# Performance work log

Hardware: AMD Instinct MI355X
Metric: run time of the kernel (lower is better)

The kernel has to match this reference:

```python
import jax, jax.numpy as jnp
import numpy as np
import math

B, S, HID = 2, 2048, 512
H, HKV, QB, VB = 8, 2, 8, 16
W = 256 // QB            # suffix window size = 32
QKD = W * QB             # unfolded qk dim = 256
TAU = 1.0


def setup_inputs() -> dict:
    key = jax.random.key(0)
    ks = jax.random.split(key, 7)
    return {
        "hidden_states": jax.random.normal(ks[0], (B, S, HID), jnp.float32),
        "Wq": jax.random.normal(ks[1], (H * QB, HID), jnp.float32) * (HID ** -0.5),
        "Wk": jax.random.normal(ks[2], (HKV * QB, HID), jnp.float32) * (HID ** -0.5),
        "Wv": jax.random.normal(ks[3], (HKV * VB, HID), jnp.float32) * (HID ** -0.5),
        "Wo": jax.random.normal(ks[4], (HID, H * VB), jnp.float32) * ((H * VB) ** -0.5),
        "v_emb0": jnp.full((H * VB,), -1e-5, jnp.float32),
        "v_emb1": jnp.full((H * VB,), +1e-5, jnp.float32),
    }


def _forward(hidden_states, Wq, Wk, Wv, Wo, v_emb0, v_emb1):
    b, s, _ = hidden_states.shape
    # bit-quantized (soft) q/k/v projections
    q = jnp.tanh((hidden_states @ Wq.T) / TAU).reshape(b, s, H, QB).transpose(0, 2, 1, 3)      # [B,H,S,QB]
    k = jnp.tanh((hidden_states @ Wk.T) / TAU).reshape(b, s, HKV, QB).transpose(0, 2, 1, 3)    # [B,HKV,S,QB]
    v = jax.nn.sigmoid((hidden_states @ Wv.T) / TAU).reshape(b, s, HKV, VB).transpose(0, 2, 1, 3)
    # suffix shift of values: F.pad(v, (0,0,-1,1)) -> v[t] <- v[t+1], last position zero
    v = jnp.concatenate([v[:, :, 1:], jnp.zeros_like(v[:, :, :1])], axis=2)                    # [B,HKV,S,VB]
    # left-pad seq by W-1 zeros, then unfold sliding windows of length W
    pad = ((0, 0), (0, 0), (W - 1, 0), (0, 0))
    qp, kp = jnp.pad(q, pad), jnp.pad(k, pad)
    win = jnp.arange(s)[:, None] + jnp.arange(W)[None, :]   # [S,W] window indices into padded seq
    qw = qp[:, :, win, :].reshape(b, H, s, QKD)             # concat window positions x bits
    kw = kp[:, :, win, :].reshape(b, HKV, s, QKD)
    # GQA: repeat kv heads
    rep = H // HKV
    kw = jnp.repeat(kw, rep, axis=1)
    vr = jnp.repeat(v, rep, axis=1)
    scale = 1.0 / math.sqrt(QKD) / TAU
    # custom bias r_j / (r_i + 1) under strictly-causal mask (j < i)
    r = jnp.arange(s, dtype=hidden_states.dtype)
    mask = jnp.tril(jnp.ones((s, s), dtype=bool), -1)
    bias = jnp.where(mask, (r[None, :] / (r[:, None] + 1.0)) / TAU, 0.0)
    scores = jnp.einsum('bhqd,bhkd->bhqk', qw, kw) * scale + bias
    neg = jnp.finfo(scores.dtype).min
    scores = jnp.where(mask, scores, neg)
    # stable masked softmax (fully-masked row 0 -> zero weights instead of NaN)
    scores = scores - jax.lax.stop_gradient(jnp.max(scores, axis=-1, keepdims=True))
    e = jnp.exp(scores) * mask
    attn = e / jnp.maximum(jnp.sum(e, axis=-1, keepdims=True), 1e-30)
    out = jnp.einsum('bhqk,bhkd->bhqd', attn, vr)           # [B,H,S,VB]
    out = out.transpose(0, 2, 1, 3).reshape(b, s, H * VB)
    # learned emb0/emb1 interpolation
    out = out * v_emb1 + (1.0 - out) * v_emb0
    return out @ Wo.T


def reference(hidden_states, Wq, Wk, Wv, Wo, v_emb0, v_emb1):
    return _forward(hidden_states, Wq, Wk, Wv, Wo, v_emb0, v_emb1)
```

## Files before the change

### kernel.cpp

```cpp
#include <hip/hip_runtime.h>
#include <hip/hip_bf16.h>

typedef unsigned int u32;
typedef unsigned short u16;
typedef float f32x4 __attribute__((ext_vector_type(4)));
typedef short s16x8 __attribute__((ext_vector_type(8)));

#define B_   2
#define S_   2048
#define HID_ 512
#define H_   8
#define HKV_ 2
#define QB_  8
#define VB_  16
#define NQ_  64
#define HVB_ 128
#define SCALE_ 0.0625f
#define MFIX_  17.0f

__device__ __forceinline__ u16 f2bf(float f) {
    u32 b = __builtin_bit_cast(u32, f);
    b += 0x7FFFu + ((b >> 16) & 1u);
    return (u16)(b >> 16);
}
__device__ __forceinline__ float bf2f(u16 h) {
    u32 b = ((u32)h) << 16;
    return __builtin_bit_cast(float, b);
}
__device__ __forceinline__ f32x4 mfma16(s16x8 a, s16x8 b, f32x4 c) {
    return __builtin_amdgcn_mfma_f32_16x16x32_bf16(a, b, c, 0, 0, 0);
}
__device__ __forceinline__ float fast_tanh(float x) {
    float e = __expf(2.f * x);
    return 1.f - 2.f * __builtin_amdgcn_rcpf(e + 1.f);
}
__device__ __forceinline__ float fast_sigmoid(float x) {
    return __builtin_amdgcn_rcpf(1.f + __expf(-x));
}

__global__ void k0_convert(const float* __restrict__ Wq, const float* __restrict__ Wk,
                           const float* __restrict__ Wv, const float* __restrict__ Wo,
                           u16* __restrict__ Wc, u16* __restrict__ Wob) {
    int idx = blockIdx.x * 256 + threadIdx.x;
    {
        int n = idx >> 9, k = idx & 511;
        float v = (n < NQ_) ? Wq[n * HID_ + k]
                : (n < NQ_ + 16) ? Wk[(n - NQ_) * HID_ + k]
                : (n < 112) ? Wv[(n - NQ_ - 16) * HID_ + k] : 0.f;
        Wc[idx] = f2bf(v);
    }
    Wob[idx] = f2bf(Wo[idx]);
}

__global__ __launch_bounds__(256) void k1_proj(
    const float* __restrict__ hidden, const u16* __restrict__ Wc,
    u16* __restrict__ qb, u16* __restrict__ kb, u16* __restrict__ vt)
{
    const int tid = threadIdx.x;
    const int r0 = blockIdx.x * 16;
    const int wv = tid >> 6, lane = tid & 63;
    const int li = lane & 15, lo4 = lane >> 4;

    const float* hrow = hidden + (r0 + li) * HID_;

    f32x4 acc[2];
    acc[0] = (f32x4){0.f, 0.f, 0.f, 0.f};
    acc[1] = (f32x4){0.f, 0.f, 0.f, 0.f};

    #pragma unroll
    for (int kc = 0; kc < 16; ++kc) {
        f32x4 x0 = *(const f32x4*)&hrow[32 * kc + 8 * lo4];
        f32x4 x1 = *(const f32x4*)&hrow[32 * kc + 8 * lo4 + 4];
        s16x8 a = { (short)f2bf(x0[0]), (short)f2bf(x0[1]), (short)f2bf(x0[2]), (short)f2bf(x0[3]),
                    (short)f2bf(x1[0]), (short)f2bf(x1[1]), (short)f2bf(x1[2]), (short)f2bf(x1[3]) };
        #pragma unroll
        for (int u = 0; u < 2; ++u) {
            int n = (wv + 4 * u) * 16 + li;
            s16x8 bfr = *(const s16x8*)&Wc[n * HID_ + 32 * kc + 8 * lo4];
            acc[u] = mfma16(a, bfr, acc[u]);
        }
    }

    #pragma unroll
    for (int u = 0; u < 2; ++u) {
        int n = (wv + 4 * u) * 16 + li;
        if (n < 112) {
            #pragma unroll
            for (int reg = 0; reg < 4; ++reg) {
                int gs = r0 + 4 * lo4 + reg;
                int b = gs >> 11, s = gs & 2047;
                float pre = acc[u][reg];
                if (n < NQ_) {
                    int h = n >> 3, bit = n & 7;
                    qb[(((b * H_ + h) * S_) + s) * QB_ + bit] = f2bf(fast_tanh(pre));
                } else if (n < NQ_ + 16) {
                    int nk = n - NQ_;
                    kb[(((b * HKV_ + (nk >> 3)) * S_) + s) * QB_ + (nk & 7)] = f2bf(fast_tanh(pre));
                } else {
                    int nv = n - NQ_ - 16;
                    int hv = nv >> 4, vb = nv & 15;
                    u16 sig = f2bf(fast_sigmoid(pre));
                    if (s > 0)
                        vt[((b * HKV_ + hv) * VB_ + vb) * S_ + (s - 1)] = sig;
                    if (s == S_ - 1)
                        vt[((b * HKV_ + hv) * VB_ + vb) * S_ + (S_ - 1)] = 0;
                }
            }
        }
    }
}

__global__ __launch_bounds__(256, 2) void k2_attn(
    const u16* __restrict__ qb, const u16* __restrict__ kb, const u16* __restrict__ vt,
    const float* __restrict__ vemb0, const float* __restrict__ vemb1,
    u16* __restrict__ AO)
{
    __shared__ __align__(16) u16 ks[2][2][96 * 8];
    __shared__ __align__(16) u16 psa[4][32 * 72];
    __shared__ __align__(16) float Om[4][2][16][17];
    __shared__ float lv[4][2][16];

    const int tid = threadIdx.x;
    const int bid = blockIdx.x;
    const int rb = bid >> 4;
    const int r  = (rb < 16) ? (31 - rb) : (rb - 16);
    const int I0 = r * 64;
    const int nJ = r + 1;
    const int bh = bid & 15;
    const int b = bh >> 3, h = bh & 7, hkv = h >> 2;

    const int qhb = ((b * H_ + h) * S_) * QB_;
    const int khb = ((b * HKV_ + hkv) * S_) * QB_;
    const int vhb = ((b * HKV_ + hkv) * VB_) * S_;

    const int w = tid >> 6, lane = tid & 63;
    const int rw = w & 1, g = w >> 1;
    const int li = lane & 15, lo4 = lane >> 4;
    const int tloc = tid & 127;

    u16* psw = psa[w];

    s16x8 qf[2][8];
    #pragma unroll
    for (int ig = 0; ig < 2; ++ig) {
        const int gr0 = I0 + 32 * rw + 16 * ig + li - 31 + lo4;
        const u16* qp = qb + qhb + gr0 * QB_;
        #pragma unroll
        for (int kk = 0; kk < 8; ++kk) {
            s16x8 v = {0, 0, 0, 0, 0, 0, 0, 0};
            if (gr0 + 4 * kk >= 0) v = *(const s16x8*)(qp + kk * 32);
            qf[ig][kk] = v;
        }
    }

    float binv[2][4];
    #pragma unroll
    for (int ig = 0; ig < 2; ++ig)
        #pragma unroll
        for (int reg = 0; reg < 4; ++reg) {
            float d = (float)(I0 + 32 * rw + 16 * ig + 4 * lo4 + reg + 1);
            float rc = __builtin_amdgcn_rcpf(d);
            binv[ig][reg] = rc * (2.f - d * rc);
        }

    f32x4 O[2];
    O[0] = (f32x4){0.f, 0.f, 0.f, 0.f};
    O[1] = (f32x4){0.f, 0.f, 0.f, 0.f};
    float lsum[2][4] = {{0.f, 0.f, 0.f, 0.f}, {0.f, 0.f, 0.f, 0.f}};

    const u16* vtp = vt + vhb + li * S_ + 8 * lo4;

    if (g < nJ && tloc < 95) {
        int gr = 64 * g - 31 + tloc;
        s16x8 v = {0, 0, 0, 0, 0, 0, 0, 0};
        if (gr >= 0) v = *(const s16x8*)(kb + khb + gr * QB_);
        *(s16x8*)&ks[g][0][tloc * 8] = v;
    }
    __syncthreads();

    const int nT = (nJ + 1) >> 1;
    for (int t = 0; t < nT; ++t) {
        const int cb = t & 1;
        const int jt = 2 * t + g;

        const bool do_stage = ((jt + 2) < nJ) && (tloc < 95);
        s16x8 stg;
        if (do_stage)
            stg = *(const s16x8*)(kb + khb + (64 * (jt + 2) - 31 + tloc) * QB_);

        if (jt < nJ) {
            const u16* kbuf = &ks[g][cb][(li + lo4) * 8];
            f32x4 sacc[2][4];
            #pragma unroll
            for (int ig = 0; ig < 2; ++ig)
                #pragma unroll
                for (int ns = 0; ns < 4; ++ns)
                    sacc[ig][ns] = (f32x4){0.f, 0.f, 0.f, 0.f};
            #pragma unroll
            for (int m = 0; m < 20; ++m) {
                s16x8 f = *(const s16x8*)(kbuf + 32 * m);
                {
                    int kk = m & 3, ns = m >> 2;
                    if (ns < 4) {
                        sacc[0][ns] = mfma16(qf[0][kk], f, sacc[0][ns]);
                        sacc[1][ns] = mfma16(qf[1][kk], f, sacc[1][ns]);
                    }
                }
                {
                    int kk = (m & 3) + 4, ns = (m >> 2) - 1;
                    if (ns >= 0) {
                        sacc[0][ns] = mfma16(qf[0][kk], f, sacc[0][ns]);
                        sacc[1][ns] = mfma16(qf[1][kk], f, sacc[1][ns]);
                    }
                }
            }

            const int J0 = jt * 64;
            int jv[4];
            #pragma unroll
            for (int ns = 0; ns < 4; ++ns) jv[ns] = J0 + 16 * ns + li;
            #pragma unroll
            for (int ig = 0; ig < 2; ++ig) {
                #pragma unroll
                for (int reg = 0; reg < 4; ++reg) {
                    const int i = I0 + 32 * rw + 16 * ig + 4 * lo4 + reg;
                    const float bi = binv[ig][reg];
                    #pragma unroll
                    for (int ns = 0; ns < 4; ++ns) {
                        float s = fmaf(sacc[ig][ns][reg], SCALE_, (float)jv[ns] * bi);
                        float p = (jv[ns] < i) ? __expf(s - MFIX_) : 0.0f;
                        lsum[ig][reg] += p;
                        psw[(ig * 16 + 4 * lo4 + reg) * 72 + 16 * ns + li] = f2bf(p);
                    }
                }
            }

            #pragma unroll
            for (int ig = 0; ig < 2; ++ig) {
                #pragma unroll
                for (int kk2 = 0; kk2 < 2; ++kk2) {
                    s16x8 pa = *(const s16x8*)&psw[(ig * 16 + li) * 72 + 32 * kk2 + 8 * lo4];
                    s16x8 pb = *(const s16x8*)(vtp + J0 + 32 * kk2);
                    O[ig] = mfma16(pa, pb, O[ig]);
                }
            }
        }

        if (do_stage)
            *(s16x8*)&ks[g][cb ^ 1][tloc * 8] = stg;

        __syncthreads();
    }

    #pragma unroll
    for (int ig = 0; ig < 2; ++ig) {
        #pragma unroll
        for (int reg = 0; reg < 4; ++reg) {
            float l = lsum[ig][reg];
            l += __shfl_xor(l, 1);
            l += __shfl_xor(l, 2);
            l += __shfl_xor(l, 4);
            l += __shfl_xor(l, 8);
            Om[w][ig][4 * lo4 + reg][li] = O[ig][reg];
            if (li == 0) lv[w][ig][4 * lo4 + reg] = l;
        }
    }
    __syncthreads();

    if (g == 0) {
        const int hc = h * VB_ + li;
        const float e0 = vemb0[hc], e1 = vemb1[hc];
        #pragma unroll
        for (int ig = 0; ig < 2; ++ig) {
            #pragma unroll
            for (int reg = 0; reg < 4; ++reg) {
                const int row = 4 * lo4 + reg;
                float Oc = Om[w][ig][row][li] + Om[w + 2][ig][row][li];
                float lc = lv[w][ig][row] + lv[w + 2][ig][row];
                float lr = fmaxf(lc, 1e-30f);
                float rinv = __builtin_amdgcn_rcpf(lr);
                rinv = rinv * (2.f - lr * rinv);
                float o = Oc * rinv;
                const int s = I0 + 32 * rw + 16 * ig + row;
                AO[(b * S_ + s) * HVB_ + hc] = f2bf(e0 + o * (e1 - e0));
            }
        }
    }
}

__global__ __launch_bounds__(256) void k3_out(
    const u16* __restrict__ AO, const u16* __restrict__ Wob,
    float* __restrict__ out)
{
    const int tid = threadIdx.x;
    const int r0 = (blockIdx.x >> 2) * 16;
    const int cg = blockIdx.x & 3;
    const int wv = tid >> 6, lane = tid & 63;
    const int li = lane & 15, lo4 = lane >> 4;

    const u16* arow = AO + (r0 + li) * HVB_;

    f32x4 acc[2];
    acc[0] = (f32x4){0.f, 0.f, 0.f, 0.f};
    acc[1] = (f32x4){0.f, 0.f, 0.f, 0.f};

    #pragma unroll
    for (int kc = 0; kc < 4; ++kc) {
        s16x8 a = *(const s16x8*)&arow[32 * kc + 8 * lo4];
        #pragma unroll
        for (int u = 0; u < 2; ++u) {
            int o = cg * 128 + (wv + 4 * u) * 16 + li;
            s16x8 bfr = *(const s16x8*)&Wob[o * HVB_ + 32 * kc + 8 * lo4];
            acc[u] = mfma16(a, bfr, acc[u]);
        }
    }

    #pragma unroll
    for (int u = 0; u < 2; ++u) {
        int o = cg * 128 + (wv + 4 * u) * 16 + li;
        #pragma unroll
        for (int reg = 0; reg < 4; ++reg)
            out[(r0 + 4 * lo4 + reg) * HID_ + o] = acc[u][reg];
    }
}

extern "C" void kernel_launch(void* const* d_in, const int* in_sizes, int n_in,
                              void* d_out, int out_size, void* d_ws, size_t ws_size,
                              hipStream_t stream)
{
    (void)in_sizes; (void)n_in; (void)out_size;
    const float* hidden = (const float*)d_in[0];
    const float* Wq = (const float*)d_in[1];
    const float* Wk = (const float*)d_in[2];
    const float* Wv = (const float*)d_in[3];
    const float* Wo = (const float*)d_in[4];
    const float* ve0 = (const float*)d_in[5];
    const float* ve1 = (const float*)d_in[6];
    float* out = (float*)d_out;

    char* base = (char*)d_ws;
    u16* qb  = (u16*)(base);
    u16* kb  = (u16*)(base + 524288);
    u16* vt  = (u16*)(base + 655360);
    u16* AO  = (u16*)(base + 917504);
    u16* Wc  = (u16*)(base + 1966080);
    u16* Wob = (u16*)(base + 2097152);
    if (ws_size < 2228224) return;

    hipLaunchKernelGGL(k0_convert, dim3(256), dim3(256), 0, stream,
                       Wq, Wk, Wv, Wo, Wc, Wob);
    hipLaunchKernelGGL(k1_proj, dim3(256), dim3(256), 0, stream,
                       hidden, Wc, qb, kb, vt);
    hipLaunchKernelGGL(k2_attn, dim3(512), dim3(256), 0, stream,
                       qb, kb, vt, ve0, ve1, AO);
    hipLaunchKernelGGL(k3_out, dim3(1024), dim3(256), 0, stream,
                       AO, Wob, out);
}
```

Before: 68.83 us.

## Split attention into 32-row blocks with 4-way key split, drop LDS K staging

The attention kernel now handles 32 query rows per block with four waves striding over key tiles, doubling the grid to 1024 blocks and raising the occupancy hint to 4. K tiles are loaded straight from global memory into registers, replacing the double-buffered shared-memory staging and its per-iteration block barriers. The 1/16 score scale is folded into the stored q values, and the bias is computed incrementally with a precomputed step. The causal mask test now runs only on diagonal tiles. The trade-offs are redundant global K loads across waves, more register pressure from holding 20 K fragments, and four partial results to combine at the end.

```diff
diff --git a/kernel.cpp b/kernel.cpp
--- a/kernel.cpp
+++ b/kernel.cpp
@@ -15,7 +15,6 @@
 #define VB_  16
 #define NQ_  64
 #define HVB_ 128
-#define SCALE_ 0.0625f
 #define MFIX_  17.0f
 
 __device__ __forceinline__ u16 f2bf(float f) {
@@ -92,7 +91,7 @@
                 float pre = acc[u][reg];
                 if (n < NQ_) {
                     int h = n >> 3, bit = n & 7;
-                    qb[(((b * H_ + h) * S_) + s) * QB_ + bit] = f2bf(fast_tanh(pre));
+                    qb[(((b * H_ + h) * S_) + s) * QB_ + bit] = f2bf(fast_tanh(pre) * 0.0625f);
                 } else if (n < NQ_ + 16) {
                     int nk = n - NQ_;
                     kb[(((b * HKV_ + (nk >> 3)) * S_) + s) * QB_ + (nk & 7)] = f2bf(fast_tanh(pre));
@@ -110,41 +109,36 @@
     }
 }
 
-__global__ __launch_bounds__(256, 2) void k2_attn(
+__global__ __launch_bounds__(256, 4) void k2_attn(
     const u16* __restrict__ qb, const u16* __restrict__ kb, const u16* __restrict__ vt,
     const float* __restrict__ vemb0, const float* __restrict__ vemb1,
     u16* __restrict__ AO)
 {
-    __shared__ __align__(16) u16 ks[2][2][96 * 8];
     __shared__ __align__(16) u16 psa[4][32 * 72];
-    __shared__ __align__(16) float Om[4][2][16][17];
+    __shared__ float Om[4][2][16][16];
     __shared__ float lv[4][2][16];
 
-    const int tid = threadIdx.x;
     const int bid = blockIdx.x;
     const int rb = bid >> 4;
-    const int r  = (rb < 16) ? (31 - rb) : (rb - 16);
-    const int I0 = r * 64;
-    const int nJ = r + 1;
+    const int r  = (rb < 32) ? (63 - rb) : (rb - 32);
+    const int I0 = r * 32;
+    const int nJ = ((I0 + 30) >> 6) + 1;
     const int bh = bid & 15;
     const int b = bh >> 3, h = bh & 7, hkv = h >> 2;
 
-    const int qhb = ((b * H_ + h) * S_) * QB_;
-    const int khb = ((b * HKV_ + hkv) * S_) * QB_;
-    const int vhb = ((b * HKV_ + hkv) * VB_) * S_;
-
-    const int w = tid >> 6, lane = tid & 63;
-    const int rw = w & 1, g = w >> 1;
+    const int g = threadIdx.x >> 6;
+    const int lane = threadIdx.x & 63;
     const int li = lane & 15, lo4 = lane >> 4;
-    const int tloc = tid & 127;
-
-    u16* psw = psa[w];
+
+    u16* psw = psa[g];
+    const u16* kpl = kb + ((b * HKV_ + hkv) * S_) * QB_ + (li + lo4 - 31) * QB_;
+    const u16* vtp = vt + ((b * HKV_ + hkv) * VB_) * S_ + li * S_ + 8 * lo4;
 
     s16x8 qf[2][8];
     #pragma unroll
     for (int ig = 0; ig < 2; ++ig) {
-        const int gr0 = I0 + 32 * rw + 16 * ig + li - 31 + lo4;
-        const u16* qp = qb + qhb + gr0 * QB_;
+        const int gr0 = I0 + 16 * ig + li - 31 + lo4;
+        const u16* qp = qb + ((b * H_ + h) * S_) * QB_ + gr0 * QB_;
         #pragma unroll
         for (int kk = 0; kk < 8; ++kk) {
             s16x8 v = {0, 0, 0, 0, 0, 0, 0, 0};
@@ -153,103 +147,103 @@
         }
     }
 
-    float binv[2][4];
-    #pragma unroll
-    for (int ig = 0; ig < 2; ++ig)
+    int ibase[2];
+    float binv[2][4], bstep[2][4];
+    #pragma unroll
+    for (int ig = 0; ig < 2; ++ig) {
+        ibase[ig] = I0 + 16 * ig + 4 * lo4;
         #pragma unroll
         for (int reg = 0; reg < 4; ++reg) {
-            float d = (float)(I0 + 32 * rw + 16 * ig + 4 * lo4 + reg + 1);
+            float d = (float)(ibase[ig] + reg + 1);
             float rc = __builtin_amdgcn_rcpf(d);
-            binv[ig][reg] = rc * (2.f - d * rc);
-        }
+            rc = rc * (2.f - d * rc);
+            binv[ig][reg] = rc;
+            bstep[ig][reg] = 16.f * rc;
+        }
+    }
 
     f32x4 O[2];
     O[0] = (f32x4){0.f, 0.f, 0.f, 0.f};
     O[1] = (f32x4){0.f, 0.f, 0.f, 0.f};
     float lsum[2][4] = {{0.f, 0.f, 0.f, 0.f}, {0.f, 0.f, 0.f, 0.f}};
 
-    const u16* vtp = vt + vhb + li * S_ + 8 * lo4;
-
-    if (g < nJ && tloc < 95) {
-        int gr = 64 * g - 31 + tloc;
-        s16x8 v = {0, 0, 0, 0, 0, 0, 0, 0};
-        if (gr >= 0) v = *(const s16x8*)(kb + khb + gr * QB_);
-        *(s16x8*)&ks[g][0][tloc * 8] = v;
-    }
-    __syncthreads();
-
-    const int nT = (nJ + 1) >> 1;
-    for (int t = 0; t < nT; ++t) {
-        const int cb = t & 1;
-        const int jt = 2 * t + g;
-
-        const bool do_stage = ((jt + 2) < nJ) && (tloc < 95);
-        s16x8 stg;
-        if (do_stage)
-            stg = *(const s16x8*)(kb + khb + (64 * (jt + 2) - 31 + tloc) * QB_);
-
-        if (jt < nJ) {
-            const u16* kbuf = &ks[g][cb][(li + lo4) * 8];
-            f32x4 sacc[2][4];
-            #pragma unroll
-            for (int ig = 0; ig < 2; ++ig)
+    for (int jt = g; jt < nJ; jt += 4) {
+        const int J0 = jt * 64;
+
+        s16x8 vfr0 = *(const s16x8*)(vtp + J0);
+        s16x8 vfr1 = *(const s16x8*)(vtp + J0 + 32);
+
+        s16x8 ld[20];
+        const u16* kt = kpl + jt * 512;
+        if (jt == 0) {
+            #pragma unroll
+            for (int m = 0; m < 20; ++m) {
+                s16x8 v = {0, 0, 0, 0, 0, 0, 0, 0};
+                if (li + lo4 + 4 * m >= 31) v = *(const s16x8*)(kt + 32 * m);
+                ld[m] = v;
+            }
+        } else {
+            #pragma unroll
+            for (int m = 0; m < 20; ++m)
+                ld[m] = *(const s16x8*)(kt + 32 * m);
+        }
+
+        f32x4 sacc[2][4];
+        #pragma unroll
+        for (int ig = 0; ig < 2; ++ig)
+            #pragma unroll
+            for (int ns = 0; ns < 4; ++ns)
+                sacc[ig][ns] = (f32x4){0.f, 0.f, 0.f, 0.f};
+        #pragma unroll
+        for (int m = 0; m < 20; ++m) {
+            s16x8 f = ld[m];
+            {
+                int kk = m & 3, ns = m >> 2;
+                if (ns < 4) {
+                    sacc[0][ns] = mfma16(qf[0][kk], f, sacc[0][ns]);
+                    sacc[1][ns] = mfma16(qf[1][kk], f, sacc[1][ns]);
+                }
+            }
+            {
+                int kk = (m & 3) + 4, ns = (m >> 2) - 1;
+                if (ns >= 0) {
+                    sacc[0][ns] = mfma16(qf[0][kk], f, sacc[0][ns]);
+                    sacc[1][ns] = mfma16(qf[1][kk], f, sacc[1][ns]);
+                }
+            }
+        }
+
+        const float jlif = (float)(J0 + li);
+        #pragma unroll
+        for (int ig = 0; ig < 2; ++ig) {
+            const bool edgev = (J0 + 63) >= (I0 + 16 * ig);
+            #pragma unroll
+            for (int reg = 0; reg < 4; ++reg) {
+                float bns = fmaf(jlif, binv[ig][reg], -MFIX_);
+                const int irow = ibase[ig] + reg;
+                float p[4];
+                #pragma unroll
+                for (int ns = 0; ns < 4; ++ns) {
+                    float e = __expf(sacc[ig][ns][reg] + bns);
+                    if (edgev)
+                        e = (J0 + 16 * ns + li < irow) ? e : 0.f;
+                    p[ns] = e;
+                    bns += bstep[ig][reg];
+                }
+                lsum[ig][reg] += (p[0] + p[1]) + (p[2] + p[3]);
                 #pragma unroll
                 for (int ns = 0; ns < 4; ++ns)
-                    sacc[ig][ns] = (f32x4){0.f, 0.f, 0.f, 0.f};
-            #pragma unroll
-            for (int m = 0; m < 20; ++m) {
-                s16x8 f = *(const s16x8*)(kbuf + 32 * m);
-                {
-                    int kk = m & 3, ns = m >> 2;
-                    if (ns < 4) {
-                        sacc[0][ns] = mfma16(qf[0][kk], f, sacc[0][ns]);
-                        sacc[1][ns] = mfma16(qf[1][kk], f, sacc[1][ns]);
-                    }
-                }
-                {
-                    int kk = (m & 3) + 4, ns = (m >> 2) - 1;
-                    if (ns >= 0) {
-                        sacc[0][ns] = mfma16(qf[0][kk], f, sacc[0][ns]);
-                        sacc[1][ns] = mfma16(qf[1][kk], f, sacc[1][ns]);
-                    }
-                }
-            }
-
-            const int J0 = jt * 64;
-            int jv[4];
-            #pragma unroll
-            for (int ns = 0; ns < 4; ++ns) jv[ns] = J0 + 16 * ns + li;
-            #pragma unroll
-            for (int ig = 0; ig < 2; ++ig) {
-                #pragma unroll
-                for (int reg = 0; reg < 4; ++reg) {
-                    const int i = I0 + 32 * rw + 16 * ig + 4 * lo4 + reg;
-                    const float bi = binv[ig][reg];
-                    #pragma unroll
-                    for (int ns = 0; ns < 4; ++ns) {
-                        float s = fmaf(sacc[ig][ns][reg], SCALE_, (float)jv[ns] * bi);
-                        float p = (jv[ns] < i) ? __expf(s - MFIX_) : 0.0f;
-                        lsum[ig][reg] += p;
-                        psw[(ig * 16 + 4 * lo4 + reg) * 72 + 16 * ns + li] = f2bf(p);
-                    }
-                }
-            }
-
-            #pragma unroll
-            for (int ig = 0; ig < 2; ++ig) {
-                #pragma unroll
-                for (int kk2 = 0; kk2 < 2; ++kk2) {
-                    s16x8 pa = *(const s16x8*)&psw[(ig * 16 + li) * 72 + 32 * kk2 + 8 * lo4];
-                    s16x8 pb = *(const s16x8*)(vtp + J0 + 32 * kk2);
-                    O[ig] = mfma16(pa, pb, O[ig]);
-                }
-            }
-        }
-
-        if (do_stage)
-            *(s16x8*)&ks[g][cb ^ 1][tloc * 8] = stg;
-
-        __syncthreads();
+                    psw[(ig * 16 + 4 * lo4 + reg) * 72 + 16 * ns + li] = f2bf(p[ns]);
+            }
+        }
+
+        #pragma unroll
+        for (int ig = 0; ig < 2; ++ig) {
+            s16x8 pa0 = *(const s16x8*)&psw[(ig * 16 + li) * 72 + 8 * lo4];
+            s16x8 pa1 = *(const s16x8*)&psw[(ig * 16 + li) * 72 + 32 + 8 * lo4];
+            O[ig] = mfma16(pa0, vfr0, O[ig]);
+            O[ig] = mfma16(pa1, vfr1, O[ig]);
+        }
     }
 
     #pragma unroll
@@ -261,8 +255,8 @@
             l += __shfl_xor(l, 2);
             l += __shfl_xor(l, 4);
             l += __shfl_xor(l, 8);
-            Om[w][ig][4 * lo4 + reg][li] = O[ig][reg];
-            if (li == 0) lv[w][ig][4 * lo4 + reg] = l;
+            Om[g][ig][4 * lo4 + reg][li] = O[ig][reg];
+            if (li == 0) lv[g][ig][4 * lo4 + reg] = l;
         }
     }
     __syncthreads();
@@ -275,13 +269,15 @@
             #pragma unroll
             for (int reg = 0; reg < 4; ++reg) {
                 const int row = 4 * lo4 + reg;
-                float Oc = Om[w][ig][row][li] + Om[w + 2][ig][row][li];
-                float lc = lv[w][ig][row] + lv[w + 2][ig][row];
+                float Oc = (Om[0][ig][row][li] + Om[1][ig][row][li])
+                         + (Om[2][ig][row][li] + Om[3][ig][row][li]);
+                float lc = (lv[0][ig][row] + lv[1][ig][row])
+                         + (lv[2][ig][row] + lv[3][ig][row]);
                 float lr = fmaxf(lc, 1e-30f);
                 float rinv = __builtin_amdgcn_rcpf(lr);
                 rinv = rinv * (2.f - lr * rinv);
                 float o = Oc * rinv;
-                const int s = I0 + 32 * rw + 16 * ig + row;
+                const int s = I0 + 16 * ig + row;
                 AO[(b * S_ + s) * HVB_ + hc] = f2bf(e0 + o * (e1 - e0));
             }
         }
@@ -351,7 +347,7 @@
                        Wq, Wk, Wv, Wo, Wc, Wob);
     hipLaunchKernelGGL(k1_proj, dim3(256), dim3(256), 0, stream,
                        hidden, Wc, qb, kb, vt);
-    hipLaunchKernelGGL(k2_attn, dim3(512), dim3(256), 0, stream,
+    hipLaunchKernelGGL(k2_attn, dim3(1024), dim3(256), 0, stream,
                        qb, kb, vt, ve0, ve1, AO);
     hipLaunchKernelGGL(k3_out, dim3(1024), dim3(256), 0, stream,
                        AO, Wob, out);
```

After: 137.9 us. +100.4%, slower.
